# Kernel tuning notes

Hardware: AMD Instinct MI355X
Metric: run time of the kernel (lower is better)

The kernel has to match this reference:

```python
import jax, jax.numpy as jnp
from jax import lax
import numpy as np

B, H, W = 1, 128, 256
C = 32           # feature_channels
D = 32           # max_disp
HID = 64         # hidden_channels in message passing
ITERS = 5


def conv2d(x, w, b):
    # x: [N, Cin, H, W], w: [Cout, Cin, kh, kw], SAME padding, stride 1
    y = lax.conv_general_dilated(x, w, (1, 1), [(1, 1), (1, 1)],
                                 dimension_numbers=('NCHW', 'OIHW', 'NCHW'))
    return y + b[None, :, None, None]


def setup_inputs() -> dict:
    key = jax.random.key(0)
    ks = jax.random.split(key, 12)
    def p(k, shape, s=0.05):
        return jax.random.normal(k, shape, jnp.float32) * s
    return {
        'left_img':  jax.random.normal(ks[0], (B, 3, H, W), jnp.float32),
        'right_img': jax.random.normal(ks[1], (B, 3, H, W), jnp.float32),
        # feature extractor (3 -> C -> C)
        'fe_w1': p(ks[2], (C, 3, 3, 3)),  'fe_b1': jnp.zeros((C,), jnp.float32),
        'fe_w2': p(ks[3], (C, C, 3, 3)),  'fe_b2': jnp.zeros((C,), jnp.float32),
        # cost volume 1x1 conv over concat(left, shifted_right): 2C -> 1
        'cv_w': p(ks[4], (2 * C,)),       'cv_b': jnp.zeros((), jnp.float32),
        # message passing: concat(feature, belief)=C+1 -> HID -> 1
        'mp_w1': p(ks[5], (HID, C + 1, 3, 3)), 'mp_b1': jnp.zeros((HID,), jnp.float32),
        'mp_w2': p(ks[6], (1, HID, 3, 3)),     'mp_b2': jnp.zeros((1,), jnp.float32),
        # refinement: concat(left_img, disparity)=4 -> 32 -> 32 -> 1 residual
        'rf_w1': p(ks[7], (32, 4, 3, 3)),  'rf_b1': jnp.zeros((32,), jnp.float32),
        'rf_w2': p(ks[8], (32, 32, 3, 3)), 'rf_b2': jnp.zeros((32,), jnp.float32),
        'rf_w3': p(ks[9], (1, 32, 3, 3)),  'rf_b3': jnp.zeros((1,), jnp.float32),
    }


def _forward(left_img, right_img, fe_w1, fe_b1, fe_w2, fe_b2, cv_w, cv_b,
             mp_w1, mp_b1, mp_w2, mp_b2, rf_w1, rf_b1, rf_w2, rf_b2, rf_w3, rf_b3):
    def feat(img):
        h = jax.nn.relu(conv2d(img, fe_w1, fe_b1))
        return jax.nn.relu(conv2d(h, fe_w2, fe_b2))

    lf = feat(left_img)    # [B, C, H, W]
    rf = feat(right_img)   # [B, C, H, W]

    # Cost volume: shift right features by each disparity, 1x1 conv on concat.
    rf_sh = jnp.stack([jnp.pad(rf, ((0, 0), (0, 0), (0, 0), (d, 0)))[..., :W]
                       for d in range(D)])                     # [D, B, C, H, W]
    pair = jnp.concatenate([jnp.broadcast_to(lf[None], rf_sh.shape), rf_sh], axis=2)  # [D,B,2C,H,W]
    cost = jnp.einsum('dbchw,c->dbhw', pair, cv_w) + cv_b      # [D, B, H, W]
    data = cost[:, :, None]                                     # [D, B, 1, H, W]

    # Iterative BP message passing, vectorized across all disparity planes.
    def mp(data_term):  # data_term: [B, 1, H, W]
        def step(belief, _):
            x = jnp.concatenate([lf, belief], axis=1)           # [B, C+1, H, W]
            hdn = jax.nn.relu(conv2d(x, mp_w1, mp_b1))          # [B, HID, H, W]
            msg = conv2d(hdn, mp_w2, mp_b2)                     # [B, 1, H, W]
            return data_term + msg, None
        belief, _ = lax.scan(step, data_term, None, length=ITERS)
        return belief

    beliefs = jax.vmap(mp)(data)                                # [D, B, 1, H, W]
    refined = jnp.transpose(beliefs, (1, 2, 0, 3, 4))           # [B, 1, D, H, W]

    prob = jax.nn.softmax(-refined, axis=2)                     # [B, 1, D, H, W]
    idx = jnp.arange(D, dtype=prob.dtype)
    disparity = jnp.einsum('bodhw,d->bohw', prob, idx)          # [B, 1, H, W]

    # Refinement network (residual).
    x = jnp.concatenate([left_img, disparity], axis=1)          # [B, 4, H, W]
    r = jax.nn.relu(conv2d(x, rf_w1, rf_b1))
    r = jax.nn.relu(conv2d(r, rf_w2, rf_b2))
    res = conv2d(r, rf_w3, rf_b3)
    return disparity + res                                      # [B, 1, H, W]


def reference(left_img, right_img, fe_w1, fe_b1, fe_w2, fe_b2, cv_w, cv_b,
              mp_w1, mp_b1, mp_w2, mp_b2, rf_w1, rf_b1, rf_w2, rf_b2, rf_w3, rf_b3):
    return _forward(left_img, right_img, fe_w1, fe_b1, fe_w2, fe_b2, cv_w, cv_b,
                    mp_w1, mp_b1, mp_w2, mp_b2, rf_w1, rf_b1, rf_w2, rf_b2, rf_w3, rf_b3)
```

## Files before the change

### kernel.cpp

```cpp
#include <hip/hip_runtime.h>
#include <hip/hip_bf16.h>

#define H 128
#define W 256
#define HW (H*W)
#define NC 32
#define ND 32
#define NHID 64

__global__ __launch_bounds__(256) void conv3x3(
        const float* __restrict__ in0, const float* __restrict__ in1,
        float* __restrict__ out0, float* __restrict__ out1,
        const float* __restrict__ w, const float* __restrict__ b,
        int CIN, int COUT, int wstride, int dorelu,
        const float* __restrict__ addin, int tpose) {
    __shared__ float tile[2][4][10][35];
    const int tid = threadIdx.x;
    const int zg = (COUT + 7) >> 3;
    const int img = blockIdx.z / zg;
    const int cog = blockIdx.z % zg;
    const float* in = img ? in1 : in0;
    float* out = img ? out1 : out0;
    const int cobase = cog * 8;
    int nco = COUT - cobase; if (nco > 8) nco = 8;
    const int gx0 = blockIdx.x * 32, gy0 = blockIdx.y * 8;
    const int tx = tid & 31, ty = tid >> 5;

    const int nst = (CIN + 3) >> 2;
    {
        int nch = CIN < 4 ? CIN : 4;
        for (int i = tid; i < nch * 340; i += 256) {
            int ch = i / 340, rem = i % 340;
            int r = rem / 34, cc = rem % 34;
            int gy = gy0 + r - 1, gx = gx0 + cc - 1;
            tile[0][ch][r][cc] = (gy >= 0 && gy < H && gx >= 0 && gx < W)
                                 ? in[(size_t)ch * HW + gy * W + gx] : 0.f;
        }
    }
    __syncthreads();

    float acc[8];
#pragma unroll
    for (int i = 0; i < 8; i++) acc[i] = 0.f;

    for (int s = 0; s < nst; s++) {
        const int c0 = s * 4;
        int nch = CIN - c0; if (nch > 4) nch = 4;
        if (s + 1 < nst) {
            const int c1 = c0 + 4;
            int nch2 = CIN - c1; if (nch2 > 4) nch2 = 4;
            const int nb = (s + 1) & 1;
            for (int i = tid; i < nch2 * 340; i += 256) {
                int ch = i / 340, rem = i % 340;
                int r = rem / 34, cc = rem % 34;
                int gy = gy0 + r - 1, gx = gx0 + cc - 1;
                tile[nb][ch][r][cc] = (gy >= 0 && gy < H && gx >= 0 && gx < W)
                                      ? in[(size_t)(c1 + ch) * HW + gy * W + gx] : 0.f;
            }
        }
        const int cb = s & 1;
        for (int ch = 0; ch < nch; ch++) {
            float v[9];
#pragma unroll
            for (int ky = 0; ky < 3; ky++)
#pragma unroll
                for (int kx = 0; kx < 3; kx++)
                    v[ky * 3 + kx] = tile[cb][ch][ty + ky][tx + kx];
            const float* wrow = w + (size_t)cobase * wstride + (size_t)(c0 + ch) * 9;
#pragma unroll
            for (int co = 0; co < 8; co++) {
                if (co < nco) {
                    const float* wp = wrow + (size_t)co * wstride;
#pragma unroll
                    for (int k = 0; k < 9; k++) acc[co] += wp[k] * v[k];
                }
            }
        }
        __syncthreads();
    }

    const int gy = gy0 + ty, gx = gx0 + tx;
    const float ad = addin ? addin[gy * W + gx] : 0.f;
    if (tpose) {
        float* op = out + (size_t)(gy * W + gx) * 64 + cobase;
#pragma unroll
        for (int co = 0; co < 8; co++) {
            float r = acc[co] + b[cobase + co];
            if (dorelu) r = fmaxf(r, 0.f);
            op[co] = r + ad;
        }
    } else {
#pragma unroll
        for (int co = 0; co < 8; co++) {
            if (co < nco) {
                float r = acc[co] + b[cobase + co];
                if (dorelu) r = fmaxf(r, 0.f);
                r += ad;
                out[(size_t)(cobase + co) * HW + gy * W + gx] = r;
            }
        }
    }
}

__global__ void chan_cost(const float* __restrict__ lf, const float* __restrict__ rf,
                          const float* __restrict__ cvw, const float* __restrict__ cvb,
                          float* __restrict__ cost, float* __restrict__ bel) {
    __shared__ float rsS[W];
    const int x = threadIdx.x;
    const int p = blockIdx.x * W + x;
    float ls = 0.f, rs = 0.f;
    for (int c = 0; c < NC; c++) {
        ls += lf[c * HW + p] * cvw[c];
        rs += rf[c * HW + p] * cvw[NC + c];
    }
    rsS[x] = rs;
    ls += cvb[0];
    __syncthreads();
#pragma unroll
    for (int d = 0; d < ND; d++) {
        float cc = ls + (x >= d ? rsS[x - d] : 0.f);
        cost[(size_t)d * HW + p] = cc;
        bel[(size_t)d * HW + p] = cc;
    }
}

#define LOADROW(YC, AR)                                                        \
  {                                                                            \
    if ((YC) >= 0 && (YC) < H) {                                               \
      AR[0] = bp[e0off];                                                       \
      _Pragma("unroll") for (int j = 1; j < 17; j++) AR[j] = bp[(j - 8) * 64]; \
      AR[17] = bp[e17off];                                                     \
    }                                                                          \
    bp += W * 64;                                                              \
  }

#define LOADBEL(Z, BR)                                                         \
  {                                                                            \
    const int z_ = (Z);                                                        \
    if (z_ >= 0 && z_ < H) {                                                   \
      const float* br_ = beld + (size_t)z_ * W + x0;                           \
      BR[0] = xnot0 ? br_[-2] : 0.f;                                           \
      BR[1] = xnot0 ? br_[-1] : 0.f;                                           \
      _Pragma("unroll") for (int q = 0; q < 16; q++) BR[q + 2] = br_[q];       \
      BR[18] = xnotE ? br_[16] : 0.f;                                          \
      BR[19] = xnotE ? br_[17] : 0.f;                                          \
    } else {                                                                   \
      _Pragma("unroll") for (int q = 0; q < 20; q++) BR[q] = 0.f;              \
    }                                                                          \
  }

#define COMPUTE(U, AR, HARR, B0, B1, B2)                                       \
  {                                                                            \
    const int yc_ = y0 + (U);                                                  \
    if (yc_ < 0 || yc_ >= H) {                                                 \
      _Pragma("unroll") for (int j = 0; j < 18; j++) HARR[j] = 0.f;            \
    } else {                                                                   \
      _Pragma("unroll") for (int j = 0; j < 18; j++) {                         \
        float acc_ = AR[j];                                                    \
        acc_ += w1[0] * B0[j] + w1[1] * B0[j + 1] + w1[2] * B0[j + 2];         \
        acc_ += w1[3] * B1[j] + w1[4] * B1[j + 1] + w1[5] * B1[j + 2];         \
        acc_ += w1[6] * B2[j] + w1[7] * B2[j + 1] + w1[8] * B2[j + 2];         \
        HARR[j] = fmaxf(acc_, 0.f);                                            \
      }                                                                        \
      if (x0 == 0) HARR[0] = 0.f;                                              \
      if (x0 == W - 16) HARR[17] = 0.f;                                        \
    }                                                                          \
  }

#define EMIT3(T, HH2, HH1, HH0)                                                \
  {                                                                            \
    _Pragma("unroll") for (int jo = 0; jo < 16; jo++) {                        \
      float pp = w2[0] * HH2[jo] + w2[1] * HH2[jo + 1] + w2[2] * HH2[jo + 2]   \
               + w2[3] * HH1[jo] + w2[4] * HH1[jo + 1] + w2[5] * HH1[jo + 2]   \
               + w2[6] * HH0[jo] + w2[7] * HH0[jo + 1] + w2[8] * HH0[jo + 2];  \
      partW[jo][lane] = pp;                                                    \
    }                                                                          \
    {                                                                          \
      const float4* pr = (const float4*)&partW[pq][qq * 16];                   \
      float cg_ = cost[obase + (size_t)(T) * W];                               \
      float4 v0 = pr[0], v1 = pr[1];                                           \
      float s_ = ((v0.x + v0.y) + (v0.z + v0.w)) +                             \
                 ((v1.x + v1.y) + (v1.z + v1.w));                              \
      float4 v2 = pr[2], v3 = pr[3];                                           \
      s_ += ((v2.x + v2.y) + (v2.z + v2.w)) +                                  \
            ((v3.x + v3.y) + (v3.z + v3.w));                                   \
      s_ += __shfl_xor(s_, 16);                                                \
      s_ += __shfl_xor(s_, 32);                                                \
      if (qq == 0) bout[obase + (size_t)(T) * W] = cg_ + s_ + b2;              \
    }                                                                          \
  }

#define STEP(T, AIN, AOUT, HX2, HX1, HX0, B0, B1, B2, BN, DOLOAD, DOBEL)       \
  {                                                                            \
    if (DOBEL) { LOADBEL(y0 + (T) + 3, BN); }                                  \
    if (DOLOAD) { LOADROW(y0 + (T) + 2, AOUT); }                               \
    COMPUTE((T) + 1, AIN, HX0, B0, B1, B2);                                    \
    EMIT3(T, HX2, HX1, HX0);                                                   \
  }

__global__ __launch_bounds__(256, 1) void mp_iter_fast(
    const float* __restrict__ At,
    const float* __restrict__ cost,
    const float* __restrict__ bin,
    float* __restrict__ bout,
    const float* __restrict__ mp_w1,
    const float* __restrict__ mp_w2,
    const float* __restrict__ mp_b2) {
    __shared__ float partS[4][16][68];

    const int tid = threadIdx.x;
    const int lane = tid & 63;
    const int lw = __builtin_amdgcn_readfirstlane(tid >> 6);
    float (*partW)[68] = partS[lw];

    const int i = blockIdx.x;
    const int xcd = i & 7;
    const int jj = i >> 3;
    const int ybl = jj & 1;
    const int sl = (jj >> 1) & 15;
    const int d4 = jj >> 5;
    const int d = d4 * 4 + lw;
    const int x0 = sl * 16;
    const int y0 = (xcd + 8 * ybl) * 8;
    const bool xnot0 = (x0 > 0), xnotE = (x0 < W - 16);

    float w1[9], w2[9];
#pragma unroll
    for (int k = 0; k < 9; k++) {
        w1[k] = mp_w1[lane * 297 + 288 + k];
        w2[k] = mp_w2[lane * 9 + k];
    }
    const float b2 = mp_b2[0];

    const float* bp = At + (size_t)(y0 - 1) * (W * 64) + (x0 + 7) * 64 + lane;
    const int e0off  = (x0 == 0)      ? -448 : -512;
    const int e17off = (x0 == W - 16) ?  512 :  576;

    const float* beld = bin + (size_t)d * HW;
    const int pq = lane & 15, qq = lane >> 4;
    const size_t obase = (size_t)d * HW + (size_t)y0 * W + x0 + pq;

    float aA[18], aB[18];
    float hA[18], hB[18], hC[18];
    float bl0[20], bl1[20], bl2[20], bl3[20];

    LOADBEL(y0 - 2, bl0);
    LOADBEL(y0 - 1, bl1);
    LOADBEL(y0,     bl2);
    LOADROW(y0 - 1, aA);
    LOADROW(y0,     aB);
    COMPUTE(-1, aA, hA, bl0, bl1, bl2);
    LOADBEL(y0 + 1, bl3);
    LOADROW(y0 + 1, aA);
    COMPUTE(0, aB, hB, bl1, bl2, bl3);
    LOADBEL(y0 + 2, bl0);

    STEP(0, aA, aB, hA, hB, hC, bl2, bl3, bl0, bl1, 1, 1)
    STEP(1, aB, aA, hB, hC, hA, bl3, bl0, bl1, bl2, 1, 1)
    STEP(2, aA, aB, hC, hA, hB, bl0, bl1, bl2, bl3, 1, 1)
    STEP(3, aB, aA, hA, hB, hC, bl1, bl2, bl3, bl0, 1, 1)
    STEP(4, aA, aB, hB, hC, hA, bl2, bl3, bl0, bl1, 1, 1)
    STEP(5, aB, aA, hC, hA, hB, bl3, bl0, bl1, bl2, 1, 1)
    STEP(6, aA, aB, hA, hB, hC, bl0, bl1, bl2, bl3, 1, 1)
    STEP(7, aB, aA, hB, hC, hA, bl1, bl2, bl3, bl0, 0, 0)
}

__global__ void softmax_disp(const float* __restrict__ bel, const float* __restrict__ left,
                             float* __restrict__ disp, float* __restrict__ x4) {
    int p = blockIdx.x * 256 + threadIdx.x;
    if (p >= HW) return;
    float v[ND];
    float m = -1e30f;
#pragma unroll
    for (int d = 0; d < ND; d++) {
        v[d] = -bel[d * HW + p];
        m = fmaxf(m, v[d]);
    }
    float s = 0.f, ws = 0.f;
#pragma unroll
    for (int d = 0; d < ND; d++) {
        float e = __expf(v[d] - m);
        s += e;
        ws += e * (float)d;
    }
    float dv = ws / s;
    disp[p] = dv;
    x4[3 * HW + p] = dv;
    x4[p] = left[p];
    x4[HW + p] = left[HW + p];
    x4[2 * HW + p] = left[2 * HW + p];
}

extern "C" void kernel_launch(void* const* d_in, const int* in_sizes, int n_in,
                              void* d_out, int out_size, void* d_ws, size_t ws_size,
                              hipStream_t stream) {
    const float* left   = (const float*)d_in[0];
    const float* right  = (const float*)d_in[1];
    const float* fe_w1  = (const float*)d_in[2];
    const float* fe_b1  = (const float*)d_in[3];
    const float* fe_w2  = (const float*)d_in[4];
    const float* fe_b2  = (const float*)d_in[5];
    const float* cv_w   = (const float*)d_in[6];
    const float* cv_b   = (const float*)d_in[7];
    const float* mp_w1  = (const float*)d_in[8];
    const float* mp_b1  = (const float*)d_in[9];
    const float* mp_w2  = (const float*)d_in[10];
    const float* mp_b2  = (const float*)d_in[11];
    const float* rf_w1  = (const float*)d_in[12];
    const float* rf_b1  = (const float*)d_in[13];
    const float* rf_w2  = (const float*)d_in[14];
    const float* rf_b2  = (const float*)d_in[15];
    const float* rf_w3  = (const float*)d_in[16];
    const float* rf_b3  = (const float*)d_in[17];
    float* out = (float*)d_out;

    float* ws = (float*)d_ws;
    float* At    = ws;
    float* tmp0  = ws;
    float* tmp1  = ws + 1048576;
    float* lf    = ws + 2097152;
    float* rfeat = ws + 3145728;
    float* cost  = ws + 4194304;
    float* bel   = ws + 5242880;
    float* bel2  = ws + 6291456;
    float* disp  = ws + 7405568;
    float* x4    = ws + 7438336;

    dim3 blk(256);

    conv3x3<<<dim3(8, 16, 8), blk, 0, stream>>>(left, right, tmp0, tmp1, fe_w1, fe_b1, 3, 32, 27, 1, nullptr, 0);
    conv3x3<<<dim3(8, 16, 8), blk, 0, stream>>>(tmp0, tmp1, lf, rfeat, fe_w2, fe_b2, 32, 32, 288, 1, nullptr, 0);

    conv3x3<<<dim3(8, 16, 8), blk, 0, stream>>>(lf, lf, At, At, mp_w1, mp_b1, 32, 64, 297, 0, nullptr, 1);

    chan_cost<<<dim3(H), blk, 0, stream>>>(lf, rfeat, cv_w, cv_b, cost, bel);

    dim3 gmp(2048);
    mp_iter_fast<<<gmp, blk, 0, stream>>>(At, cost, bel,  bel2, mp_w1, mp_w2, mp_b2);
    mp_iter_fast<<<gmp, blk, 0, stream>>>(At, cost, bel2, bel,  mp_w1, mp_w2, mp_b2);
    mp_iter_fast<<<gmp, blk, 0, stream>>>(At, cost, bel,  bel2, mp_w1, mp_w2, mp_b2);
    mp_iter_fast<<<gmp, blk, 0, stream>>>(At, cost, bel2, bel,  mp_w1, mp_w2, mp_b2);
    mp_iter_fast<<<gmp, blk, 0, stream>>>(At, cost, bel,  bel2, mp_w1, mp_w2, mp_b2);

    softmax_disp<<<dim3(HW / 256), blk, 0, stream>>>(bel2, left, disp, x4);

    conv3x3<<<dim3(8, 16, 4), blk, 0, stream>>>(x4, x4, At, At, rf_w1, rf_b1, 4, 32, 36, 1, nullptr, 0);
    conv3x3<<<dim3(8, 16, 4), blk, 0, stream>>>(At, At, rfeat, rfeat, rf_w2, rf_b2, 32, 32, 288, 1, nullptr, 0);
    conv3x3<<<dim3(8, 16, 1), blk, 0, stream>>>(rfeat, rfeat, out, out, rf_w3, rf_b3, 32, 1, 288, 0, disp, 0);
}
```

Before: 539.8 us.

## Software-pipeline message-passing row reduction and halve conv output-channel grouping

The message-passing kernel now double-buffers its per-wave shared partial-sum buffer. The LDS read-back and reduction of row T-1 are issued before row T+1's compute, so shared-memory latency overlaps with the arithmetic. Separately, the conv3x3 kernel is templated on output channels per block and launched with 4 instead of 8, which doubles the grid to raise parallelism. The trade-off is more redundant input tile loads per conv and extra registers and LDS in the message-passing kernel.

```diff
diff --git a/kernel.cpp b/kernel.cpp
--- a/kernel.cpp
+++ b/kernel.cpp
@@ -8,6 +8,7 @@
 #define ND 32
 #define NHID 64
 
+template<int NCO>
 __global__ __launch_bounds__(256) void conv3x3(
         const float* __restrict__ in0, const float* __restrict__ in1,
         float* __restrict__ out0, float* __restrict__ out1,
@@ -16,13 +17,13 @@
         const float* __restrict__ addin, int tpose) {
     __shared__ float tile[2][4][10][35];
     const int tid = threadIdx.x;
-    const int zg = (COUT + 7) >> 3;
+    const int zg = (COUT + NCO - 1) / NCO;
     const int img = blockIdx.z / zg;
     const int cog = blockIdx.z % zg;
     const float* in = img ? in1 : in0;
     float* out = img ? out1 : out0;
-    const int cobase = cog * 8;
-    int nco = COUT - cobase; if (nco > 8) nco = 8;
+    const int cobase = cog * NCO;
+    int nco = COUT - cobase; if (nco > NCO) nco = NCO;
     const int gx0 = blockIdx.x * 32, gy0 = blockIdx.y * 8;
     const int tx = tid & 31, ty = tid >> 5;
 
@@ -39,9 +40,9 @@
     }
     __syncthreads();
 
-    float acc[8];
-#pragma unroll
-    for (int i = 0; i < 8; i++) acc[i] = 0.f;
+    float acc[NCO];
+#pragma unroll
+    for (int i = 0; i < NCO; i++) acc[i] = 0.f;
 
     for (int s = 0; s < nst; s++) {
         const int c0 = s * 4;
@@ -68,7 +69,7 @@
                     v[ky * 3 + kx] = tile[cb][ch][ty + ky][tx + kx];
             const float* wrow = w + (size_t)cobase * wstride + (size_t)(c0 + ch) * 9;
 #pragma unroll
-            for (int co = 0; co < 8; co++) {
+            for (int co = 0; co < NCO; co++) {
                 if (co < nco) {
                     const float* wp = wrow + (size_t)co * wstride;
 #pragma unroll
@@ -84,14 +85,16 @@
     if (tpose) {
         float* op = out + (size_t)(gy * W + gx) * 64 + cobase;
 #pragma unroll
-        for (int co = 0; co < 8; co++) {
-            float r = acc[co] + b[cobase + co];
-            if (dorelu) r = fmaxf(r, 0.f);
-            op[co] = r + ad;
+        for (int co = 0; co < NCO; co++) {
+            if (co < nco) {
+                float r = acc[co] + b[cobase + co];
+                if (dorelu) r = fmaxf(r, 0.f);
+                op[co] = r + ad;
+            }
         }
     } else {
 #pragma unroll
-        for (int co = 0; co < 8; co++) {
+        for (int co = 0; co < NCO; co++) {
             if (co < nco) {
                 float r = acc[co] + b[cobase + co];
                 if (dorelu) r = fmaxf(r, 0.f);
@@ -167,35 +170,42 @@
     }                                                                          \
   }
 
-#define EMIT3(T, HH2, HH1, HH0)                                                \
+#define WRITES(T, HM, H0, HP)                                                  \
   {                                                                            \
     _Pragma("unroll") for (int jo = 0; jo < 16; jo++) {                        \
-      float pp = w2[0] * HH2[jo] + w2[1] * HH2[jo + 1] + w2[2] * HH2[jo + 2]   \
-               + w2[3] * HH1[jo] + w2[4] * HH1[jo + 1] + w2[5] * HH1[jo + 2]   \
-               + w2[6] * HH0[jo] + w2[7] * HH0[jo + 1] + w2[8] * HH0[jo + 2];  \
-      partW[jo][lane] = pp;                                                    \
+      float pp = w2[0] * HM[jo] + w2[1] * HM[jo + 1] + w2[2] * HM[jo + 2]      \
+               + w2[3] * H0[jo] + w2[4] * H0[jo + 1] + w2[5] * H0[jo + 2]      \
+               + w2[6] * HP[jo] + w2[7] * HP[jo + 1] + w2[8] * HP[jo + 2];     \
+      partW[(T) & 1][jo][lane] = pp;                                           \
     }                                                                          \
-    {                                                                          \
-      const float4* pr = (const float4*)&partW[pq][qq * 16];                   \
-      float cg_ = cost[obase + (size_t)(T) * W];                               \
-      float4 v0 = pr[0], v1 = pr[1];                                           \
-      float s_ = ((v0.x + v0.y) + (v0.z + v0.w)) +                             \
-                 ((v1.x + v1.y) + (v1.z + v1.w));                              \
-      float4 v2 = pr[2], v3 = pr[3];                                           \
-      s_ += ((v2.x + v2.y) + (v2.z + v2.w)) +                                  \
-            ((v3.x + v3.y) + (v3.z + v3.w));                                   \
-      s_ += __shfl_xor(s_, 16);                                                \
-      s_ += __shfl_xor(s_, 32);                                                \
-      if (qq == 0) bout[obase + (size_t)(T) * W] = cg_ + s_ + b2;              \
-    }                                                                          \
-  }
-
-#define STEP(T, AIN, AOUT, HX2, HX1, HX0, B0, B1, B2, BN, DOLOAD, DOBEL)       \
+  }
+
+#define RISSUE(T)                                                              \
+  {                                                                            \
+    rvc = cost[obase + (size_t)(T) * W];                                       \
+    const float4* pr_ = (const float4*)&partW[(T) & 1][pq][qq * 16];           \
+    rv0 = pr_[0]; rv1 = pr_[1]; rv2 = pr_[2]; rv3 = pr_[3];                    \
+  }
+
+#define RFINISH(T)                                                             \
+  {                                                                            \
+    float s_ = (((rv0.x + rv0.y) + (rv0.z + rv0.w)) +                          \
+                ((rv1.x + rv1.y) + (rv1.z + rv1.w))) +                         \
+               (((rv2.x + rv2.y) + (rv2.z + rv2.w)) +                          \
+                ((rv3.x + rv3.y) + (rv3.z + rv3.w)));                          \
+    s_ += __shfl_xor(s_, 16);                                                  \
+    s_ += __shfl_xor(s_, 32);                                                  \
+    if (qq == 0) bout[obase + (size_t)(T) * W] = rvc + s_ + b2;                \
+  }
+
+#define STEPG(T, AIN, AOUT, HX2, HX1, HX0, B0, B1, B2, BN, DOLOAD, DOBEL)      \
   {                                                                            \
     if (DOBEL) { LOADBEL(y0 + (T) + 3, BN); }                                  \
     if (DOLOAD) { LOADROW(y0 + (T) + 2, AOUT); }                               \
+    RISSUE((T) - 1);                                                           \
     COMPUTE((T) + 1, AIN, HX0, B0, B1, B2);                                    \
-    EMIT3(T, HX2, HX1, HX0);                                                   \
+    WRITES(T, HX2, HX1, HX0);                                                  \
+    RFINISH((T) - 1);                                                          \
   }
 
 __global__ __launch_bounds__(256, 1) void mp_iter_fast(
@@ -206,12 +216,12 @@
     const float* __restrict__ mp_w1,
     const float* __restrict__ mp_w2,
     const float* __restrict__ mp_b2) {
-    __shared__ float partS[4][16][68];
+    __shared__ float partS[4][2][16][68];
 
     const int tid = threadIdx.x;
     const int lane = tid & 63;
     const int lw = __builtin_amdgcn_readfirstlane(tid >> 6);
-    float (*partW)[68] = partS[lw];
+    float (*partW)[16][68] = partS[lw];
 
     const int i = blockIdx.x;
     const int xcd = i & 7;
@@ -243,6 +253,8 @@
     float aA[18], aB[18];
     float hA[18], hB[18], hC[18];
     float bl0[20], bl1[20], bl2[20], bl3[20];
+    float4 rv0, rv1, rv2, rv3;
+    float rvc;
 
     LOADBEL(y0 - 2, bl0);
     LOADBEL(y0 - 1, bl1);
@@ -254,15 +266,19 @@
     LOADROW(y0 + 1, aA);
     COMPUTE(0, aB, hB, bl1, bl2, bl3);
     LOADBEL(y0 + 2, bl0);
-
-    STEP(0, aA, aB, hA, hB, hC, bl2, bl3, bl0, bl1, 1, 1)
-    STEP(1, aB, aA, hB, hC, hA, bl3, bl0, bl1, bl2, 1, 1)
-    STEP(2, aA, aB, hC, hA, hB, bl0, bl1, bl2, bl3, 1, 1)
-    STEP(3, aB, aA, hA, hB, hC, bl1, bl2, bl3, bl0, 1, 1)
-    STEP(4, aA, aB, hB, hC, hA, bl2, bl3, bl0, bl1, 1, 1)
-    STEP(5, aB, aA, hC, hA, hB, bl3, bl0, bl1, bl2, 1, 1)
-    STEP(6, aA, aB, hA, hB, hC, bl0, bl1, bl2, bl3, 1, 1)
-    STEP(7, aB, aA, hB, hC, hA, bl1, bl2, bl3, bl0, 0, 0)
+    LOADROW(y0 + 2, aB);
+    COMPUTE(1, aA, hC, bl2, bl3, bl0);
+    WRITES(0, hA, hB, hC);
+    LOADBEL(y0 + 3, bl1);
+    STEPG(1, aB, aA, hB, hC, hA, bl3, bl0, bl1, bl2, 1, 1)
+    STEPG(2, aA, aB, hC, hA, hB, bl0, bl1, bl2, bl3, 1, 1)
+    STEPG(3, aB, aA, hA, hB, hC, bl1, bl2, bl3, bl0, 1, 1)
+    STEPG(4, aA, aB, hB, hC, hA, bl2, bl3, bl0, bl1, 1, 1)
+    STEPG(5, aB, aA, hC, hA, hB, bl3, bl0, bl1, bl2, 1, 1)
+    STEPG(6, aA, aB, hA, hB, hC, bl0, bl1, bl2, bl3, 1, 1)
+    STEPG(7, aB, aA, hB, hC, hA, bl1, bl2, bl3, bl0, 0, 0)
+    RISSUE(7);
+    RFINISH(7);
 }
 
 __global__ void softmax_disp(const float* __restrict__ bel, const float* __restrict__ left,
@@ -328,10 +344,10 @@
 
     dim3 blk(256);
 
-    conv3x3<<<dim3(8, 16, 8), blk, 0, stream>>>(left, right, tmp0, tmp1, fe_w1, fe_b1, 3, 32, 27, 1, nullptr, 0);
-    conv3x3<<<dim3(8, 16, 8), blk, 0, stream>>>(tmp0, tmp1, lf, rfeat, fe_w2, fe_b2, 32, 32, 288, 1, nullptr, 0);
-
-    conv3x3<<<dim3(8, 16, 8), blk, 0, stream>>>(lf, lf, At, At, mp_w1, mp_b1, 32, 64, 297, 0, nullptr, 1);
+    conv3x3<4><<<dim3(8, 16, 16), blk, 0, stream>>>(left, right, tmp0, tmp1, fe_w1, fe_b1, 3, 32, 27, 1, nullptr, 0);
+    conv3x3<4><<<dim3(8, 16, 16), blk, 0, stream>>>(tmp0, tmp1, lf, rfeat, fe_w2, fe_b2, 32, 32, 288, 1, nullptr, 0);
+
+    conv3x3<4><<<dim3(8, 16, 16), blk, 0, stream>>>(lf, lf, At, At, mp_w1, mp_b1, 32, 64, 297, 0, nullptr, 1);
 
     chan_cost<<<dim3(H), blk, 0, stream>>>(lf, rfeat, cv_w, cv_b, cost, bel);
 
@@ -344,7 +360,7 @@
 
     softmax_disp<<<dim3(HW / 256), blk, 0, stream>>>(bel2, left, disp, x4);
 
-    conv3x3<<<dim3(8, 16, 4), blk, 0, stream>>>(x4, x4, At, At, rf_w1, rf_b1, 4, 32, 36, 1, nullptr, 0);
-    conv3x3<<<dim3(8, 16, 4), blk, 0, stream>>>(At, At, rfeat, rfeat, rf_w2, rf_b2, 32, 32, 288, 1, nullptr, 0);
-    conv3x3<<<dim3(8, 16, 1), blk, 0, stream>>>(rfeat, rfeat, out, out, rf_w3, rf_b3, 32, 1, 288, 0, disp, 0);
-}
+    conv3x3<4><<<dim3(8, 16, 8), blk, 0, stream>>>(x4, x4, At, At, rf_w1, rf_b1, 4, 32, 36, 1, nullptr, 0);
+    conv3x3<4><<<dim3(8, 16, 8), blk, 0, stream>>>(At, At, rfeat, rfeat, rf_w2, rf_b2, 32, 32, 288, 1, nullptr, 0);
+    conv3x3<4><<<dim3(8, 16, 1), blk, 0, stream>>>(rfeat, rfeat, out, out, rf_w3, rf_b3, 32, 1, 288, 0, disp, 0);
+}
```

Result: faster. 503.0 us (-6.8%).
